# Kernel tuning notes

Hardware: AMD Instinct MI355X
Metric: run time of the kernel (lower is better)

Reference implementation:

```python
import jax, jax.numpy as jnp
import numpy as np

B, C, N = 16, 128, 2048
M = 1024
NUM_BINS = 4
BOUND = [1.2, 1.0, 0.8]  # interior bin boundaries (num_bins-1 values)


def setup_inputs() -> dict:
    key = jax.random.key(0)
    k1, k2, k3, k4, k5 = jax.random.split(key, 5)
    s = 1.0 / np.sqrt(C)
    x = jax.random.normal(k1, (B, C, N), jnp.float32)
    Wq = jax.random.normal(k2, (C, C), jnp.float32) * s
    Wk = jax.random.normal(k3, (C, C), jnp.float32) * s
    Wv = jax.random.normal(k4, (C, C), jnp.float32) * s
    bin_tokens = jax.random.normal(k5, (1, C, NUM_BINS), jnp.float32) * s
    return {"x": x, "Wq": Wq, "Wk": Wk, "Wv": Wv, "bin_tokens": bin_tokens}


def _forward(x, Wq, Wk, Wv, bin_tokens):
    Bb, Cc, Nn = x.shape
    nb = bin_tokens.shape[-1]
    toks = jnp.broadcast_to(bin_tokens, (Bb, Cc, nb))
    x_tok = jnp.concatenate([x, toks], axis=2)            # (B,C,N+nb)
    # 1x1 convs (bias=False) == channel matmuls; single head (H=1)
    q = jnp.einsum('oc,bcn->bno', Wq, x)[:, None]         # (B,1,N,dq)
    k = jnp.einsum('oc,bcn->bon', Wk, x_tok)[:, None]     # (B,1,dk,N+nb)
    v = jnp.einsum('oc,bcn->bon', Wv, x_tok)[:, None]     # (B,1,dv,N+nb)
    scale = jnp.sqrt(jnp.asarray(q.shape[-1], jnp.float32))
    energy = jnp.einsum('bhnd,bhdm->bhnm', q, k) / scale  # (B,1,N,N+nb)
    attn = jax.nn.softmax(energy, axis=-1)
    attn_points = attn[..., :Nn]                          # (B,1,N,N)
    attn_bins_pre = energy[..., Nn:]                      # (B,1,N,nb) pre-softmax token scores
    # idx_mode == 'col_sum': attention score per point = column sum
    score = jnp.sum(attn_points, axis=-2)                 # (B,1,N)
    # static bin partition (dynamic_boundaries disabled)
    upper = jnp.asarray([np.inf] + BOUND, jnp.float32)
    lower = jnp.asarray(BOUND + [-np.inf], jnp.float32)
    mask = (score[..., None] < upper) & (score[..., None] >= lower)  # (B,1,N,nb)
    maskf = mask.astype(jnp.float32)
    # bin weights ('mean_relu'): masked mean of token attention, then relu
    counts = jnp.sum(maskf, axis=2)                       # (B,1,nb)
    w_pre = jnp.sum(attn_bins_pre * maskf, axis=2) / (counts + 1e-8)
    bin_w = jax.nn.relu(w_pre[:, 0])                      # (B,nb)
    max_pts = jnp.sum(mask[:, 0].astype(jnp.int32), axis=1)  # (B,nb)
    # points per bin: proportional allocation clipped to capacity, remainder
    # filled greedily in bin order (deterministic, capacity-respecting)
    p = bin_w / jnp.maximum(jnp.sum(bin_w, axis=1, keepdims=True), 1e-8)
    k0 = jnp.minimum(jnp.floor(p * M).astype(jnp.int32), max_pts)
    deficit = M - jnp.sum(k0, axis=1, keepdims=True)      # >= 0
    cap = max_pts - k0
    cum = jnp.cumsum(cap, axis=1) - cap                   # exclusive cumsum
    extra = jnp.clip(deficit - cum, 0, cap)
    k_bins = k0 + extra                                   # (B,nb), rows sum to M
    # top-k_bins per bin by attention score ('topk' sample mode)
    s = score[:, 0]                                       # (B,N)
    s_b = jnp.where(mask[:, 0], s[:, :, None], -jnp.inf)  # (B,N,nb)
    order = jnp.argsort(-s_b, axis=1)
    ranks = jnp.argsort(order, axis=1)                    # rank within each bin
    selected = mask[:, 0] & (ranks < k_bins[:, None, :])  # (B,N,nb)
    sel_any = jnp.any(selected, axis=-1)                  # (B,N), exactly M true
    _, idx = jax.lax.top_k(sel_any.astype(jnp.float32), M)  # (B,M)
    index_down = idx[:, None, :]                          # (B,H=1,M)
    # gather selected attention rows and aggregate values
    idx_e = jnp.broadcast_to(index_down[..., None], (Bb, 1, M, attn.shape[-1]))
    attn_down = jnp.take_along_axis(attn, idx_e, axis=2)  # (B,1,M,N+nb)
    v_down = jnp.einsum('bhmk,bhdk->bhmd', attn_down, v)  # (B,1,M,dv)
    x_ds = v_down.transpose(0, 2, 1, 3).reshape(Bb, M, -1).transpose(0, 2, 1)  # (B,C,M)
    return x_ds, index_down


def reference(x, Wq, Wk, Wv, bin_tokens):
    return _forward(x, Wq, Wk, Wv, bin_tokens)
```

## Files before the change

### kernel.cpp

```cpp
#include <hip/hip_runtime.h>

#define BB 16
#define CC 128
#define NN 2048
#define MM2 2052
#define VST 2056
#define XTR 2056
#define MM 1024

constexpr float RSQRT_C = 0.08838834764831845f;

typedef unsigned short u16;
typedef __attribute__((ext_vector_type(8))) short bf16x8;
typedef __attribute__((ext_vector_type(8))) _Float16 f16x8;
typedef __attribute__((ext_vector_type(4))) float f32x4;

__device__ inline u16 f2b_rn(float f) {
  unsigned u = __float_as_uint(f);
  unsigned r = u + 0x7fffu + ((u >> 16) & 1u);
  return (u16)(r >> 16);
}
__device__ inline float b2f(u16 h) { return __uint_as_float(((unsigned)h) << 16); }
__device__ inline u16 f2h(float f) {
  union { _Float16 h; u16 u; } cv; cv.h = (_Float16)f; return cv.u;
}

constexpr size_t SZ_Q  = (size_t)BB*NN*CC*2;
constexpr size_t SZ_K  = (size_t)BB*MM2*CC*2;
constexpr size_t SZ_V  = (size_t)BB*CC*VST*2;
constexpr size_t oQH = 0;
constexpr size_t oQL = oQH + SZ_Q;
constexpr size_t oKH = oQL + SZ_Q;
constexpr size_t oKL = oKH + SZ_K;
constexpr size_t oVF = oKL + SZ_K;
constexpr size_t oRS0 = oVF + SZ_V;
constexpr size_t oEB  = oRS0 + (size_t)2*BB*NN*4;
constexpr size_t oSC0 = oEB  + (size_t)BB*NN*16;
constexpr size_t oSCORE = oSC0 + (size_t)2*BB*NN*4;
constexpr size_t oBIN = oSCORE + (size_t)BB*NN*4;
constexpr size_t oKB  = oBIN + (size_t)BB*NN*4;
constexpr size_t oFL  = oKB  + 256;
constexpr size_t oIDX = oFL  + (size_t)BB*NN*4;
constexpr size_t oXH  = oIDX + (size_t)BB*MM*4;
constexpr size_t oXL  = oXH  + (size_t)BB*XTR*CC*2;
constexpr size_t oWH  = oXL  + (size_t)BB*XTR*CC*2;
constexpr size_t oWL  = oWH  + (size_t)3*CC*CC*2;
constexpr size_t oPU  = oXH;
constexpr size_t SZ_PU = (size_t)BB*NN*VST*2;
constexpr size_t oOP  = oPU + SZ_PU;
constexpr size_t SZ_OP1 = (size_t)BB*CC*MM*4;

__global__ __launch_bounds__(256) void splitX_kernel(
    const float* __restrict__ x, const float* __restrict__ bt,
    u16* __restrict__ XH, u16* __restrict__ XL)
{
  const int t = threadIdx.x;
  const int b  = blockIdx.x / 33;
  const int nt = blockIdx.x % 33;
  if (nt == 32) {
    for (int i = t; i < 4*128; i += 256) {
      int j = i >> 7, c = i & 127;
      float v = bt[c*4 + j];
      u16 hb = f2b_rn(v);
      size_t oi = ((size_t)b*XTR + NN + j)*CC + c;
      XH[oi] = hb; XL[oi] = f2b_rn(v - b2f(hb));
    }
    return;
  }
  __shared__ float xs[128][65];
  const int n0 = nt*64;
  for (int i = t; i < 128*64; i += 256) {
    int c = i >> 6, n = i & 63;
    xs[c][n] = x[((size_t)b*CC + c)*NN + n0 + n];
  }
  __syncthreads();
  for (int i = t; i < 64*128; i += 256) {
    int m = i >> 7, c = i & 127;
    float v = xs[c][m];
    u16 hb = f2b_rn(v);
    size_t oi = ((size_t)b*XTR + n0 + m)*CC + c;
    XH[oi] = hb; XL[oi] = f2b_rn(v - b2f(hb));
  }
}

__global__ __launch_bounds__(256) void splitW_kernel(
    const float* __restrict__ Wq, const float* __restrict__ Wk, const float* __restrict__ Wv,
    u16* __restrict__ WH, u16* __restrict__ WL)
{
  int i = blockIdx.x*256 + threadIdx.x;
  int w = i >> 14, rest = i & 16383;
  const float* W = (w == 0) ? Wq : (w == 1) ? Wk : Wv;
  float v = W[rest];
  u16 hb = f2b_rn(v);
  WH[i] = hb; WL[i] = f2b_rn(v - b2f(hb));
}

__global__ __launch_bounds__(256) void projM_kernel(
    const u16* __restrict__ XH, const u16* __restrict__ XL,
    const u16* __restrict__ WHs, const u16* __restrict__ WLs,
    u16* __restrict__ QH, u16* __restrict__ QL,
    u16* __restrict__ KH, u16* __restrict__ KL,
    u16* __restrict__ VF)
{
  __shared__ u16 xsh[64*128], xsl[64*128];
  const int t = threadIdx.x;
  const int b  = blockIdx.x / 33;
  const int mt = blockIdx.x % 33;
  const int m0 = mt*64;
  const int wv = t >> 6, lane = t & 63;
  const int l15 = lane & 15, lhi = lane >> 4;

  {
    const int row0 = t >> 4, chunk = t & 15;
    #pragma unroll
    for (int ii=0; ii<4; ++ii) {
      int r = row0 + ii*16; int gm = m0 + r;
      int dst = r*256 + ((chunk*16) ^ ((r&7)<<4));
      uint4 vh = make_uint4(0,0,0,0), vl = make_uint4(0,0,0,0);
      if (gm < MM2) {
        size_t g = ((size_t)b*XTR + gm)*CC + chunk*8;
        vh = *(const uint4*)(XH + g);
        vl = *(const uint4*)(XL + g);
      }
      *(uint4*)((char*)xsh + dst) = vh;
      *(uint4*)((char*)xsl + dst) = vl;
    }
  }
  __syncthreads();

  for (int w = (m0 >= NN) ? 1 : 0; w < 2; ++w) {
    const u16* whp = WHs + (size_t)w*CC*CC;
    const u16* wlp = WLs + (size_t)w*CC*CC;
    u16* OH = w ? KH : QH;
    u16* OL = w ? KL : QL;
    const float scl = w ? 1.0f : RSQRT_C;
    const int mlim = w ? MM2 : NN;
    for (int osub = 0; osub < 2; ++osub) {
      const int ocol = wv*32 + osub*16;
      bf16x8 wbh[4], wbl[4];
      #pragma unroll
      for (int it=0; it<4; ++it) {
        size_t wi = (size_t)(ocol + l15)*CC + it*32 + lhi*8;
        wbh[it] = *(const bf16x8*)(whp + wi);
        wbl[it] = *(const bf16x8*)(wlp + wi);
      }
      for (int msub = 0; msub < 4; ++msub) {
        const int mrow = msub*16 + l15;
        f32x4 acc = {0.f,0.f,0.f,0.f};
        #pragma unroll
        for (int it=0; it<4; ++it) {
          int byt = mrow*256 + ((it*64 + lhi*16) ^ ((mrow&7)<<4));
          bf16x8 ah = *(const bf16x8*)((const char*)xsh + byt);
          bf16x8 al = *(const bf16x8*)((const char*)xsl + byt);
          acc = __builtin_amdgcn_mfma_f32_16x16x32_bf16(ah, wbh[it], acc, 0,0,0);
          acc = __builtin_amdgcn_mfma_f32_16x16x32_bf16(ah, wbl[it], acc, 0,0,0);
          acc = __builtin_amdgcn_mfma_f32_16x16x32_bf16(al, wbh[it], acc, 0,0,0);
        }
        #pragma unroll
        for (int r=0;r<4;++r) {
          int m = m0 + msub*16 + lhi*4 + r;
          if (m < mlim) {
            float vv = acc[r] * scl;
            u16 hb = f2b_rn(vv);
            size_t oi = w ? ((size_t)b*MM2 + m)*CC + ocol + l15
                          : ((size_t)b*NN  + m)*CC + ocol + l15;
            OH[oi] = hb;
            OL[oi] = f2b_rn(vv - b2f(hb));
          }
        }
      }
    }
  }

  {
    const u16* whp = WHs + (size_t)2*CC*CC;
    const u16* wlp = WLs + (size_t)2*CC*CC;
    for (int osub = 0; osub < 2; ++osub) {
      const int ocol = wv*32 + osub*16;
      bf16x8 wbh[4], wbl[4];
      #pragma unroll
      for (int it=0; it<4; ++it) {
        size_t wi = (size_t)(ocol + l15)*CC + it*32 + lhi*8;
        wbh[it] = *(const bf16x8*)(whp + wi);
        wbl[it] = *(const bf16x8*)(wlp + wi);
      }
      for (int msub = 0; msub < 4; ++msub) {
        const int mrow = msub*16 + l15;
        f32x4 acc = {0.f,0.f,0.f,0.f};
        #pragma unroll
        for (int it=0; it<4; ++it) {
          int byt = mrow*256 + ((it*64 + lhi*16) ^ ((mrow&7)<<4));
          bf16x8 ah = *(const bf16x8*)((const char*)xsh + byt);
          bf16x8 al = *(const bf16x8*)((const char*)xsl + byt);
          acc = __builtin_amdgcn_mfma_f32_16x16x32_bf16(wbh[it], ah, acc, 0,0,0);
          acc = __builtin_amdgcn_mfma_f32_16x16x32_bf16(wbh[it], al, acc, 0,0,0);
          acc = __builtin_amdgcn_mfma_f32_16x16x32_bf16(wbl[it], ah, acc, 0,0,0);
        }
        #pragma unroll
        for (int r=0;r<4;++r) {
          int o = ocol + lhi*4 + r;
          int m = m0 + msub*16 + l15;
          if (m < VST)
            VF[((size_t)b*CC + o)*VST + m] = f2h(acc[r]);
        }
      }
    }
  }
}

__global__ __launch_bounds__(256) void statsA_kernel(
    const u16* __restrict__ QH, const u16* __restrict__ QL,
    const u16* __restrict__ KH, const u16* __restrict__ KL,
    float* __restrict__ rsumP, float* __restrict__ ebins)
{
  __shared__ u16 kh[64*128], kl[64*128];
  const int t = threadIdx.x;
  const int half = blockIdx.x & 1;
  const int rest = blockIdx.x >> 1;
  const int b = rest >> 5;
  const int n0 = (rest & 31) * 64;
  const int wv = t >> 6, lane = t & 63;
  const int l15 = lane & 15, lhi = lane >> 4;
  const int nw = n0 + wv*16;
  const int ktBeg = half ? 17 : 0;
  const int ktEnd = half ? 33 : 17;

  bf16x8 qh[4], ql[4];
  {
    const size_t rb = ((size_t)b*NN + nw + l15)*CC + lhi*8;
    #pragma unroll
    for (int it=0; it<4; ++it) {
      qh[it] = *(const bf16x8*)(QH + rb + it*32);
      ql[it] = *(const bf16x8*)(QL + rb + it*32);
    }
  }
  float runsum[4] = {0.f, 0.f, 0.f, 0.f};

  for (int kt = ktBeg; kt < ktEnd; ++kt) {
    const int m0 = kt*64;
    __syncthreads();
    {
      const int row0 = t >> 4, chunk = t & 15;
      #pragma unroll
      for (int ii=0; ii<4; ++ii) {
        int r = row0 + ii*16; int gm = m0 + r;
        int dst = r*256 + ((chunk*16) ^ ((r&7)<<4));
        uint4 vh = make_uint4(0,0,0,0), vl = make_uint4(0,0,0,0);
        if (gm < MM2) {
          size_t g = ((size_t)b*MM2 + gm)*CC + chunk*8;
          vh = *(const uint4*)(KH + g);
          vl = *(const uint4*)(KL + g);
        }
        *(uint4*)((char*)kh + dst) = vh;
        *(uint4*)((char*)kl + dst) = vl;
      }
    }
    __syncthreads();
    const int mcEnd = (kt == 32) ? 1 : 4;
    for (int mc = 0; mc < mcEnd; ++mc) {
      f32x4 acc = {0.f,0.f,0.f,0.f};
      const int mrow = mc*16 + l15;
      #pragma unroll
      for (int it=0; it<4; ++it) {
        int byt = mrow*256 + ((it*64 + lhi*16) ^ ((mrow&7)<<4));
        bf16x8 bh = *(const bf16x8*)((const char*)kh + byt);
        bf16x8 bl = *(const bf16x8*)((const char*)kl + byt);
        acc = __builtin_amdgcn_mfma_f32_16x16x32_bf16(qh[it], bh, acc, 0,0,0);
        acc = __builtin_amdgcn_mfma_f32_16x16x32_bf16(qh[it], bl, acc, 0,0,0);
        acc = __builtin_amdgcn_mfma_f32_16x16x32_bf16(ql[it], bh, acc, 0,0,0);
      }
      const int m = m0 + mrow;
      if (kt == 32 && l15 < 4) {
        #pragma unroll
        for (int r=0;r<4;++r)
          ebins[((size_t)b*NN + nw + lhi*4 + r)*4 + l15] = acc[r];
      }
      const bool valid = (m < MM2);
      #pragma unroll
      for (int r=0;r<4;++r)
        runsum[r] += valid ? __expf(acc[r]) : 0.f;
    }
  }
  #pragma unroll
  for (int r=0;r<4;++r) {
    runsum[r] += __shfl_xor(runsum[r], 1);
    runsum[r] += __shfl_xor(runsum[r], 2);
    runsum[r] += __shfl_xor(runsum[r], 4);
    runsum[r] += __shfl_xor(runsum[r], 8);
  }
  if (l15 == 0) {
    float* rs = rsumP + (size_t)half*BB*NN;
    #pragma unroll
    for (int r=0;r<4;++r)
      rs[(size_t)b*NN + nw + lhi*4 + r] = runsum[r];
  }
}

__global__ __launch_bounds__(256) void passP_kernel(
    const u16* __restrict__ QH, const u16* __restrict__ QL,
    const u16* __restrict__ KH, const u16* __restrict__ KL,
    const float* __restrict__ rsumP, float* __restrict__ scoreP,
    u16* __restrict__ PU)
{
  __shared__ u16 qsh[64*128], qsl[64*128];
  __shared__ float sirs[64];
  const int t = threadIdx.x;
  const int half = blockIdx.x & 1;
  const int rest = blockIdx.x >> 1;
  const int b = rest / 33;
  const int mt = rest % 33;
  const int m0 = mt * 64;
  const int wv = t >> 6, lane = t & 63;
  const int l15 = lane & 15, lhi = lane >> 4;
  const int mcol = m0 + wv*16 + l15;
  const int ntBeg = half ? 16 : 0;
  const int ntEnd = half ? 32 : 16;

  bf16x8 kbh[4], kbl[4];
  {
    const int krow = (mcol < MM2) ? mcol : (MM2-1);
    const size_t rb = ((size_t)b*MM2 + krow)*CC + lhi*8;
    #pragma unroll
    for (int it=0; it<4; ++it) {
      kbh[it] = *(const bf16x8*)(KH + rb + it*32);
      kbl[it] = *(const bf16x8*)(KL + rb + it*32);
    }
  }
  float sacc = 0.f;

  for (int nt = ntBeg; nt < ntEnd; ++nt) {
    const int n0 = nt*64;
    __syncthreads();
    {
      const int row0 = t >> 4, chunk = t & 15;
      #pragma unroll
      for (int ii=0; ii<4; ++ii) {
        int r = row0 + ii*16;
        int dst = r*256 + ((chunk*16) ^ ((r&7)<<4));
        size_t g = ((size_t)b*NN + n0 + r)*CC + chunk*8;
        *(uint4*)((char*)qsh + dst) = *(const uint4*)(QH + g);
        *(uint4*)((char*)qsl + dst) = *(const uint4*)(QL + g);
      }
      if (t < 64) {
        size_t ri = (size_t)b*NN + n0 + t;
        sirs[t] = 1.0f / (rsumP[ri] + rsumP[(size_t)BB*NN + ri]);
      }
    }
    __syncthreads();
    for (int sub = 0; sub < 4; ++sub) {
      f32x4 acc = {0.f,0.f,0.f,0.f};
      const int arow = sub*16 + l15;
      #pragma unroll
      for (int it=0; it<4; ++it) {
        int byt = arow*256 + ((it*64 + lhi*16) ^ ((arow&7)<<4));
        bf16x8 ah = *(const bf16x8*)((const char*)qsh + byt);
        bf16x8 al = *(const bf16x8*)((const char*)qsl + byt);
        acc = __builtin_amdgcn_mfma_f32_16x16x32_bf16(ah, kbh[it], acc, 0,0,0);
        acc = __builtin_amdgcn_mfma_f32_16x16x32_bf16(ah, kbl[it], acc, 0,0,0);
        acc = __builtin_amdgcn_mfma_f32_16x16x32_bf16(al, kbh[it], acc, 0,0,0);
      }
      #pragma unroll
      for (int r=0;r<4;++r) {
        int nl = sub*16 + lhi*4 + r;
        float p = __expf(acc[r]) * sirs[nl];
        if (mcol < VST)
          PU[((size_t)b*NN + n0 + nl)*VST + mcol] = f2h((mcol < MM2) ? p : 0.f);
        sacc += p;
      }
    }
  }
  sacc += __shfl_xor(sacc, 16);
  sacc += __shfl_xor(sacc, 32);
  if (lhi == 0 && mcol < NN)
    scoreP[(size_t)half*BB*NN + (size_t)b*NN + mcol] = sacc;
}

__global__ __launch_bounds__(256) void bin_kernel(
    const float* __restrict__ scoreP, const float* __restrict__ ebins,
    float* __restrict__ score, int* __restrict__ binof, int* __restrict__ kbins)
{
  const int b = blockIdx.x, t = threadIdx.x;
  float wsm[4] = {0.f,0.f,0.f,0.f};
  int   cnt[4] = {0,0,0,0};
  for (int n = t; n < NN; n += 256) {
    size_t si = (size_t)b*NN + n;
    float s = scoreP[si] + scoreP[(size_t)BB*NN + si];
    score[si] = s;
    int j = (s >= 1.2f) ? 0 : (s >= 1.0f) ? 1 : (s >= 0.8f) ? 2 : 3;
    binof[si] = j;
    wsm[j] += ebins[si*4 + j];
    cnt[j] += 1;
  }
  #pragma unroll
  for (int j=0;j<4;j++){
    for (int off=1; off<64; off<<=1){
      wsm[j] += __shfl_xor(wsm[j], off);
      cnt[j] += __shfl_xor(cnt[j], off);
    }
  }
  __shared__ float wred[4][4];
  __shared__ int   cred[4][4];
  int wave = t >> 6, lane = t & 63;
  if (lane == 0) for (int j=0;j<4;j++){ wred[wave][j]=wsm[j]; cred[wave][j]=cnt[j]; }
  __syncthreads();
  if (t == 0) {
    float wsum[4]; int cs[4];
    for (int j=0;j<4;j++){
      wsum[j]=wred[0][j]+wred[1][j]+wred[2][j]+wred[3][j];
      cs[j]=cred[0][j]+cred[1][j]+cred[2][j]+cred[3][j];
    }
    float bw[4]; float sbw = 0.f;
    for (int j=0;j<4;j++){
      float wp = wsum[j] / ((float)cs[j] + 1e-8f);
      bw[j] = fmaxf(wp, 0.f); sbw += bw[j];
    }
    float den = fmaxf(sbw, 1e-8f);
    int k0[4]; int sk0 = 0;
    for (int j=0;j<4;j++){
      float p = bw[j] / den;
      int kk = (int)floorf(p * 1024.0f);
      if (kk > cs[j]) kk = cs[j];
      k0[j]=kk; sk0 += kk;
    }
    int deficit = 1024 - sk0;
    int cum = 0;
    for (int j=0;j<4;j++){
      int cap = cs[j] - k0[j];
      int ex = deficit - cum; if (ex < 0) ex = 0; if (ex > cap) ex = cap;
      kbins[b*4+j] = k0[j] + ex;
      cum += cap;
    }
  }
}

__global__ __launch_bounds__(256) void topk_kernel(
    const float* __restrict__ score, const int* __restrict__ binof,
    const int* __restrict__ kbins, int* __restrict__ flags)
{
  __shared__ unsigned long long arr[2048];
  const int t = threadIdx.x;
  const int b = blockIdx.x >> 2;
  const int j = blockIdx.x & 3;
  for (int n = t; n < NN; n += 256) {
    unsigned long long comp = 0ull;
    if (binof[(size_t)b*NN+n] == j) {
      unsigned int bits = __float_as_uint(score[(size_t)b*NN+n]);
      bits = (bits & 0x80000000u) ? ~bits : (bits | 0x80000000u);
      comp = ((unsigned long long)bits << 32) |
             (unsigned long long)(0xFFFFFFFFu - (unsigned)n);
    }
    arr[n] = ~comp;
  }
  __syncthreads();
  for (int ksz = 2; ksz <= 2048; ksz <<= 1) {
    for (int jsz = ksz >> 1; jsz > 0; jsz >>= 1) {
      for (int i = t; i < 2048; i += 256) {
        int ixj = i ^ jsz;
        if (ixj > i) {
          unsigned long long a = arr[i], bv = arr[ixj];
          bool up = ((i & ksz) == 0);
          if ((a > bv) == up) { arr[i] = bv; arr[ixj] = a; }
        }
      }
      __syncthreads();
    }
  }
  const int kb = kbins[b*4+j];
  for (int i = t; i < kb; i += 256) {
    unsigned long long comp = ~arr[i];
    int n = (int)(0xFFFFFFFFu - (unsigned)(comp & 0xFFFFFFFFull));
    flags[(size_t)b*NN + n] = 1;
  }
}

__global__ __launch_bounds__(256) void scan_kernel(
    const int* __restrict__ flags, int* __restrict__ idxl, float* __restrict__ outIdx)
{
  __shared__ int tsum[256];
  const int b = blockIdx.x, t = threadIdx.x;
  int f[8]; int c8 = 0;
  const int base = t * 8;
  #pragma unroll
  for (int i=0;i<8;i++){ f[i] = flags[(size_t)b*NN + base + i]; c8 += f[i]; }
  tsum[t] = c8;
  __syncthreads();
  for (int off=1; off<256; off<<=1) {
    int v = (t >= off) ? tsum[t-off] : 0;
    __syncthreads();
    tsum[t] += v;
    __syncthreads();
  }
  int pos = tsum[t] - c8;
  #pragma unroll
  for (int i=0;i<8;i++){
    if (f[i] && pos < MM) {
      idxl[(size_t)b*MM + pos] = base + i;
      outIdx[(size_t)b*MM + pos] = (float)(base + i);
      pos++;
    }
  }
}

__global__ __launch_bounds__(256) void outC_kernel(
    const u16* __restrict__ PU, const u16* __restrict__ VF,
    const int* __restrict__ idxl, float* __restrict__ oPart)
{
  __shared__ u16 psh[64*64];
  __shared__ u16 vsh[128*64];
  __shared__ int rid[64];
  const int t = threadIdx.x;
  const int third = blockIdx.x % 3;
  const int rest  = blockIdx.x / 3;
  const int b  = rest >> 4;
  const int s0 = (rest & 15) * 64;
  const int wv = t >> 6, lane = t & 63;
  const int l15 = lane & 15, lhi = lane >> 4;
  const int ktBeg = third * 11, ktEnd = ktBeg + 11;

  if (t < 64) rid[t] = idxl[(size_t)b*MM + s0 + t];

  f32x4 oacc[8];
  #pragma unroll
  for (int ct=0; ct<8; ++ct) oacc[ct] = (f32x4){0.f,0.f,0.f,0.f};

  for (int kt = ktBeg; kt < ktEnd; ++kt) {
    const int m0 = kt*64;
    __syncthreads();
    #pragma unroll
    for (int ii=0; ii<2; ++ii) {
      int item = t + 256*ii;
      int row = item >> 3, ch = item & 7;
      int gm = m0 + ch*8;
      uint4 v = make_uint4(0,0,0,0);
      if (gm < VST) v = *(const uint4*)(PU + ((size_t)b*NN + rid[row])*VST + gm);
      *(uint4*)((char*)psh + row*128 + ((ch*16) ^ ((row&7)<<4))) = v;
    }
    #pragma unroll
    for (int ii=0; ii<4; ++ii) {
      int item = t + 256*ii;
      int c = item >> 3, ch = item & 7;
      int gm = m0 + ch*8;
      uint4 v = make_uint4(0,0,0,0);
      if (gm < VST) v = *(const uint4*)(VF + ((size_t)b*CC + c)*VST + gm);
      *(uint4*)((char*)vsh + c*128 + ((ch*16) ^ ((c&7)<<4))) = v;
    }
    __syncthreads();
    #pragma unroll
    for (int ki=0; ki<2; ++ki) {
      const int prow = wv*16 + l15;
      f16x8 pa = *(const f16x8*)((const char*)psh + prow*128 + ((ki*64 + lhi*16) ^ ((prow&7)<<4)));
      #pragma unroll
      for (int ct=0; ct<8; ++ct) {
        int c = ct*16 + l15;
        f16x8 vb = *(const f16x8*)((const char*)vsh + c*128 + ((ki*64 + lhi*16) ^ ((c&7)<<4)));
        oacc[ct] = __builtin_amdgcn_mfma_f32_16x16x32_f16(pa, vb, oacc[ct], 0,0,0);
      }
    }
  }
  float* op = oPart + (size_t)third*BB*CC*MM;
  #pragma unroll
  for (int ct=0; ct<8; ++ct) {
    #pragma unroll
    for (int r=0;r<4;++r) {
      op[((size_t)b*CC + ct*16 + l15)*MM + s0 + wv*16 + lhi*4 + r] = oacc[ct][r];
    }
  }
}

__global__ __launch_bounds__(256) void merge_kernel(
    const float* __restrict__ oPart, float* __restrict__ out0)
{
  const size_t i = ((size_t)blockIdx.x*256 + threadIdx.x)*4;
  const float4 a = *(const float4*)(oPart + i);
  const float4 b = *(const float4*)(oPart + (size_t)BB*CC*MM + i);
  const float4 c = *(const float4*)(oPart + (size_t)2*BB*CC*MM + i);
  float4 o;
  o.x = a.x + b.x + c.x;
  o.y = a.y + b.y + c.y;
  o.z = a.z + b.z + c.z;
  o.w = a.w + b.w + c.w;
  *(float4*)(out0 + i) = o;
}

extern "C" void kernel_launch(void* const* d_in, const int* in_sizes, int n_in,
                              void* d_out, int out_size, void* d_ws, size_t ws_size,
                              hipStream_t stream) {
  const float* x  = (const float*)d_in[0];
  const float* Wq = (const float*)d_in[1];
  const float* Wk = (const float*)d_in[2];
  const float* Wv = (const float*)d_in[3];
  const float* bt = (const float*)d_in[4];
  float* out = (float*)d_out;
  char* ws = (char*)d_ws;

  u16* QH = (u16*)(ws + oQH);
  u16* QL = (u16*)(ws + oQL);
  u16* KH = (u16*)(ws + oKH);
  u16* KL = (u16*)(ws + oKL);
  u16* VF = (u16*)(ws + oVF);
  float* rsumP = (float*)(ws + oRS0);
  float* ebins = (float*)(ws + oEB);
  float* scoreP= (float*)(ws + oSC0);
  float* score = (float*)(ws + oSCORE);
  int* binof = (int*)(ws + oBIN);
  int* kbins = (int*)(ws + oKB);
  int* flags = (int*)(ws + oFL);
  int* idxl  = (int*)(ws + oIDX);
  u16* XH = (u16*)(ws + oXH);
  u16* XL = (u16*)(ws + oXL);
  u16* WHs = (u16*)(ws + oWH);
  u16* WLs = (u16*)(ws + oWL);
  u16* PU  = (u16*)(ws + oPU);
  float* oPart = (float*)(ws + oOP);

  float* out0   = out;
  float* outIdx = out + (size_t)BB*CC*MM;

  (void)hipMemsetAsync(flags, 0, (size_t)BB*NN*sizeof(int), stream);

  hipLaunchKernelGGL(splitX_kernel,  dim3(528),  dim3(256), 0, stream, x, bt, XH, XL);
  hipLaunchKernelGGL(splitW_kernel,  dim3(192),  dim3(256), 0, stream, Wq, Wk, Wv, WHs, WLs);
  hipLaunchKernelGGL(projM_kernel,   dim3(528),  dim3(256), 0, stream, XH, XL, WHs, WLs, QH, QL, KH, KL, VF);
  hipLaunchKernelGGL(statsA_kernel,  dim3(1024), dim3(256), 0, stream, QH, QL, KH, KL, rsumP, ebins);
  hipLaunchKernelGGL(passP_kernel,   dim3(1056), dim3(256), 0, stream, QH, QL, KH, KL, rsumP, scoreP, PU);
  hipLaunchKernelGGL(bin_kernel,     dim3(16),   dim3(256), 0, stream, scoreP, ebins, score, binof, kbins);
  hipLaunchKernelGGL(topk_kernel,    dim3(64),   dim3(256), 0, stream, score, binof, kbins, flags);
  hipLaunchKernelGGL(scan_kernel,    dim3(16),   dim3(256), 0, stream, flags, idxl, outIdx);
  hipLaunchKernelGGL(outC_kernel,    dim3(768),  dim3(256), 0, stream, PU, VF, idxl, oPart);
  hipLaunchKernelGGL(merge_kernel,   dim3(2048), dim3(256), 0, stream, oPart, out0);
}
```

Before: 383.7 us.

## Store unnormalized exp scores in stats pass and defer softmax normalization

```diff
diff --git a/kernel.cpp b/kernel.cpp
--- a/kernel.cpp
+++ b/kernel.cpp
@@ -36,7 +36,7 @@
 constexpr size_t oRS0 = oVF + SZ_V;
 constexpr size_t oEB  = oRS0 + (size_t)2*BB*NN*4;
 constexpr size_t oSC0 = oEB  + (size_t)BB*NN*16;
-constexpr size_t oSCORE = oSC0 + (size_t)2*BB*NN*4;
+constexpr size_t oSCORE = oSC0 + (size_t)8*BB*NN*4;
 constexpr size_t oBIN = oSCORE + (size_t)BB*NN*4;
 constexpr size_t oKB  = oBIN + (size_t)BB*NN*4;
 constexpr size_t oFL  = oKB  + 256;
@@ -48,7 +48,6 @@
 constexpr size_t oPU  = oXH;
 constexpr size_t SZ_PU = (size_t)BB*NN*VST*2;
 constexpr size_t oOP  = oPU + SZ_PU;
-constexpr size_t SZ_OP1 = (size_t)BB*CC*MM*4;
 
 __global__ __launch_bounds__(256) void splitX_kernel(
     const float* __restrict__ x, const float* __restrict__ bt,
@@ -208,10 +207,10 @@
   }
 }
 
-__global__ __launch_bounds__(256) void statsA_kernel(
+__global__ __launch_bounds__(256) void fusedE_kernel(
     const u16* __restrict__ QH, const u16* __restrict__ QL,
     const u16* __restrict__ KH, const u16* __restrict__ KL,
-    float* __restrict__ rsumP, float* __restrict__ ebins)
+    float* __restrict__ rsumP, float* __restrict__ ebins, u16* __restrict__ PU)
 {
   __shared__ u16 kh[64*128], kl[64*128];
   const int t = threadIdx.x;
@@ -277,8 +276,12 @@
       }
       const bool valid = (m < MM2);
       #pragma unroll
-      for (int r=0;r<4;++r)
-        runsum[r] += valid ? __expf(acc[r]) : 0.f;
+      for (int r=0;r<4;++r) {
+        float ex = valid ? __expf(acc[r]) : 0.f;
+        if (m < VST)
+          PU[((size_t)b*NN + nw + lhi*4 + r)*VST + m] = f2h(ex);
+        runsum[r] += ex;
+      }
     }
   }
   #pragma unroll
@@ -296,83 +299,35 @@
   }
 }
 
-__global__ __launch_bounds__(256) void passP_kernel(
-    const u16* __restrict__ QH, const u16* __restrict__ QL,
-    const u16* __restrict__ KH, const u16* __restrict__ KL,
-    const float* __restrict__ rsumP, float* __restrict__ scoreP,
-    u16* __restrict__ PU)
-{
-  __shared__ u16 qsh[64*128], qsl[64*128];
-  __shared__ float sirs[64];
+__global__ __launch_bounds__(256) void colsum_kernel(
+    const u16* __restrict__ PU, const float* __restrict__ rsumP,
+    float* __restrict__ scoreP)
+{
+  __shared__ float sirs[256];
   const int t = threadIdx.x;
-  const int half = blockIdx.x & 1;
-  const int rest = blockIdx.x >> 1;
-  const int b = rest / 33;
-  const int mt = rest % 33;
-  const int m0 = mt * 64;
-  const int wv = t >> 6, lane = t & 63;
-  const int l15 = lane & 15, lhi = lane >> 4;
-  const int mcol = m0 + wv*16 + l15;
-  const int ntBeg = half ? 16 : 0;
-  const int ntEnd = half ? 32 : 16;
-
-  bf16x8 kbh[4], kbl[4];
+  const int blk = blockIdx.x;
+  const int ns = blk & 7;
+  const int mt = (blk >> 3) & 3;
+  const int b  = blk >> 5;
+  const int n0 = ns*256;
+  const int m0 = mt*512;
   {
-    const int krow = (mcol < MM2) ? mcol : (MM2-1);
-    const size_t rb = ((size_t)b*MM2 + krow)*CC + lhi*8;
-    #pragma unroll
-    for (int it=0; it<4; ++it) {
-      kbh[it] = *(const bf16x8*)(KH + rb + it*32);
-      kbl[it] = *(const bf16x8*)(KL + rb + it*32);
-    }
-  }
-  float sacc = 0.f;
-
-  for (int nt = ntBeg; nt < ntEnd; ++nt) {
-    const int n0 = nt*64;
-    __syncthreads();
-    {
-      const int row0 = t >> 4, chunk = t & 15;
-      #pragma unroll
-      for (int ii=0; ii<4; ++ii) {
-        int r = row0 + ii*16;
-        int dst = r*256 + ((chunk*16) ^ ((r&7)<<4));
-        size_t g = ((size_t)b*NN + n0 + r)*CC + chunk*8;
-        *(uint4*)((char*)qsh + dst) = *(const uint4*)(QH + g);
-        *(uint4*)((char*)qsl + dst) = *(const uint4*)(QL + g);
-      }
-      if (t < 64) {
-        size_t ri = (size_t)b*NN + n0 + t;
-        sirs[t] = 1.0f / (rsumP[ri] + rsumP[(size_t)BB*NN + ri]);
-      }
-    }
-    __syncthreads();
-    for (int sub = 0; sub < 4; ++sub) {
-      f32x4 acc = {0.f,0.f,0.f,0.f};
-      const int arow = sub*16 + l15;
-      #pragma unroll
-      for (int it=0; it<4; ++it) {
-        int byt = arow*256 + ((it*64 + lhi*16) ^ ((arow&7)<<4));
-        bf16x8 ah = *(const bf16x8*)((const char*)qsh + byt);
-        bf16x8 al = *(const bf16x8*)((const char*)qsl + byt);
-        acc = __builtin_amdgcn_mfma_f32_16x16x32_bf16(ah, kbh[it], acc, 0,0,0);
-        acc = __builtin_amdgcn_mfma_f32_16x16x32_bf16(ah, kbl[it], acc, 0,0,0);
-        acc = __builtin_amdgcn_mfma_f32_16x16x32_bf16(al, kbh[it], acc, 0,0,0);
-      }
-      #pragma unroll
-      for (int r=0;r<4;++r) {
-        int nl = sub*16 + lhi*4 + r;
-        float p = __expf(acc[r]) * sirs[nl];
-        if (mcol < VST)
-          PU[((size_t)b*NN + n0 + nl)*VST + mcol] = f2h((mcol < MM2) ? p : 0.f);
-        sacc += p;
-      }
-    }
-  }
-  sacc += __shfl_xor(sacc, 16);
-  sacc += __shfl_xor(sacc, 32);
-  if (lhi == 0 && mcol < NN)
-    scoreP[(size_t)half*BB*NN + (size_t)b*NN + mcol] = sacc;
+    size_t ri = (size_t)b*NN + n0 + t;
+    sirs[t] = 1.0f / (rsumP[ri] + rsumP[(size_t)BB*NN + ri]);
+  }
+  __syncthreads();
+  float s0a = 0.f, s1a = 0.f;
+  const u16* base = PU + ((size_t)b*NN + n0)*VST + m0 + 2*t;
+  #pragma unroll 4
+  for (int n = 0; n < 256; ++n) {
+    unsigned pv = *(const unsigned*)(base + (size_t)n*VST);
+    union { unsigned u; _Float16 h[2]; } cv; cv.u = pv;
+    float w = sirs[n];
+    s0a = fmaf((float)cv.h[0], w, s0a);
+    s1a = fmaf((float)cv.h[1], w, s1a);
+  }
+  float2 o; o.x = s0a; o.y = s1a;
+  *(float2*)(scoreP + (size_t)ns*BB*NN + (size_t)b*NN + m0 + 2*t) = o;
 }
 
 __global__ __launch_bounds__(256) void bin_kernel(
@@ -384,7 +339,9 @@
   int   cnt[4] = {0,0,0,0};
   for (int n = t; n < NN; n += 256) {
     size_t si = (size_t)b*NN + n;
-    float s = scoreP[si] + scoreP[(size_t)BB*NN + si];
+    float s = 0.f;
+    #pragma unroll
+    for (int h = 0; h < 8; ++h) s += scoreP[(size_t)h*BB*NN + si];
     score[si] = s;
     int j = (s >= 1.2f) ? 0 : (s >= 1.0f) ? 1 : (s >= 0.8f) ? 2 : 3;
     binof[si] = j;
@@ -503,11 +460,13 @@
 
 __global__ __launch_bounds__(256) void outC_kernel(
     const u16* __restrict__ PU, const u16* __restrict__ VF,
+    const float* __restrict__ rsumP,
     const int* __restrict__ idxl, float* __restrict__ oPart)
 {
   __shared__ u16 psh[64*64];
   __shared__ u16 vsh[128*64];
   __shared__ int rid[64];
+  __shared__ float ssel[64];
   const int t = threadIdx.x;
   const int third = blockIdx.x % 3;
   const int rest  = blockIdx.x / 3;
@@ -517,7 +476,12 @@
   const int l15 = lane & 15, lhi = lane >> 4;
   const int ktBeg = third * 11, ktEnd = ktBeg + 11;
 
-  if (t < 64) rid[t] = idxl[(size_t)b*MM + s0 + t];
+  if (t < 64) {
+    int n = idxl[(size_t)b*MM + s0 + t];
+    rid[t] = n;
+    size_t ri = (size_t)b*NN + n;
+    ssel[t] = 1.0f / (rsumP[ri] + rsumP[(size_t)BB*NN + ri]);
+  }
 
   f32x4 oacc[8];
   #pragma unroll
@@ -562,7 +526,8 @@
   for (int ct=0; ct<8; ++ct) {
     #pragma unroll
     for (int r=0;r<4;++r) {
-      op[((size_t)b*CC + ct*16 + l15)*MM + s0 + wv*16 + lhi*4 + r] = oacc[ct][r];
+      op[((size_t)b*CC + ct*16 + l15)*MM + s0 + wv*16 + lhi*4 + r] =
+          oacc[ct][r] * ssel[wv*16 + lhi*4 + r];
     }
   }
 }
@@ -621,11 +586,11 @@
   hipLaunchKernelGGL(splitX_kernel,  dim3(528),  dim3(256), 0, stream, x, bt, XH, XL);
   hipLaunchKernelGGL(splitW_kernel,  dim3(192),  dim3(256), 0, stream, Wq, Wk, Wv, WHs, WLs);
   hipLaunchKernelGGL(projM_kernel,   dim3(528),  dim3(256), 0, stream, XH, XL, WHs, WLs, QH, QL, KH, KL, VF);
-  hipLaunchKernelGGL(statsA_kernel,  dim3(1024), dim3(256), 0, stream, QH, QL, KH, KL, rsumP, ebins);
-  hipLaunchKernelGGL(passP_kernel,   dim3(1056), dim3(256), 0, stream, QH, QL, KH, KL, rsumP, scoreP, PU);
+  hipLaunchKernelGGL(fusedE_kernel,  dim3(1024), dim3(256), 0, stream, QH, QL, KH, KL, rsumP, ebins, PU);
+  hipLaunchKernelGGL(colsum_kernel,  dim3(512),  dim3(256), 0, stream, PU, rsumP, scoreP);
   hipLaunchKernelGGL(bin_kernel,     dim3(16),   dim3(256), 0, stream, scoreP, ebins, score, binof, kbins);
   hipLaunchKernelGGL(topk_kernel,    dim3(64),   dim3(256), 0, stream, score, binof, kbins, flags);
   hipLaunchKernelGGL(scan_kernel,    dim3(16),   dim3(256), 0, stream, flags, idxl, outIdx);
-  hipLaunchKernelGGL(outC_kernel,    dim3(768),  dim3(256), 0, stream, PU, VF, idxl, oPart);
+  hipLaunchKernelGGL(outC_kernel,    dim3(768),  dim3(256), 0, stream, PU, VF, rsumP, idxl, oPart);
   hipLaunchKernelGGL(merge_kernel,   dim3(2048), dim3(256), 0, stream, oPart, out0);
 }
```

Measured after the change: 325.2 us. -15.3%, faster.
